# Performance work log

Measured on AMD Instinct MI355X. Metric: run time of the kernel, lower is better.

## Reference

```python
import jax, jax.numpy as jnp
import numpy as np

B, T, C = 16, 512, 32
W = 128            # max_window
SERIES_LEN = 100000
WIN_MIN, WIN_MAX = 2.0, 64.0
SHARP = 1.0        # fixed sharpness of the soft window edge
BN_EPS = 1e-5


def setup_inputs() -> dict:
    key = jax.random.key(0)
    ks = jax.random.split(key, 6)
    x = jax.random.normal(ks[0], (B, T, C), jnp.float32)
    full_series = jax.random.normal(ks[1], (SERIES_LEN, C), jnp.float32)
    # starts >= W so the lookback window never needs padding; end = start + T
    starts = jax.random.randint(ks[2], (B,), W, SERIES_LEN - T)
    indices = jnp.stack([starts, starts + T], axis=1).astype(jnp.int32)  # (B, 2)
    # raw (logit-space) per-channel window sizes, as in the torch init
    raw_win_mean = jax.random.normal(ks[3], (C,), jnp.float32)
    raw_win_std = jax.random.normal(ks[4], (C,), jnp.float32)
    return dict(
        x=x, full_series=full_series, indices=indices,
        raw_win_mean=raw_win_mean, raw_win_std=raw_win_std,
        gamma_mean=jnp.ones((C,), jnp.float32), beta_mean=jnp.zeros((C,), jnp.float32),
        gamma_std=jnp.ones((C,), jnp.float32), beta_std=jnp.zeros((C,), jnp.float32),
    )


def _soft_window_weights(raw_win):
    # sigmoid-mapped window size in [WIN_MIN, WIN_MAX], per channel
    win = WIN_MIN + jax.nn.sigmoid(raw_win) * (WIN_MAX - WIN_MIN)          # (C,)
    age = jnp.arange(W, dtype=jnp.float32)[::-1]                            # slot W-1 is most recent (age 0)
    w = jax.nn.sigmoid(SHARP * (win[None, :] - age[:, None]))               # (W, C)
    return w


def _rolling_windows(full_series, starts):
    # batch_windows[b] = full_series[starts[b]-W : starts[b]+T]   -> (B, W+T, C)
    offs = jnp.arange(W + T)
    bw = full_series[(starts - W)[:, None] + offs[None, :]]                 # (B, W+T, C)
    # window for output step t covers slots [t, t+W) (the W points before the current step)
    tidx = jnp.arange(T)[:, None] + jnp.arange(W)[None, :]                  # (T, W)
    return bw[:, tidx, :]                                                   # (B, T, W, C)


def _batchnorm(f, gamma, beta):
    # BatchNorm1d over (B, C, T): normalize per channel over batch and time, biased var
    mean = f.mean(axis=(0, 1))
    var = ((f - mean) ** 2).mean(axis=(0, 1))
    return (f - mean) * jax.lax.rsqrt(var + BN_EPS) * gamma + beta


def reference(x, full_series, indices, raw_win_mean, raw_win_std,
              gamma_mean, beta_mean, gamma_std, beta_std):
    starts = indices[:, 0]
    xw = _rolling_windows(full_series, starts)                              # (B, T, W, C)

    # feature 1: soft-window weighted mean
    w1 = _soft_window_weights(raw_win_mean)                                 # (W, C)
    s1 = jnp.sum(w1, axis=0)                                                # (C,)
    f_mean = jnp.einsum('btwc,wc->btc', xw, w1) / s1                        # (B, T, C)

    # feature 2: soft-window weighted std
    w2 = _soft_window_weights(raw_win_std)
    s2 = jnp.sum(w2, axis=0)
    m2 = jnp.einsum('btwc,wc->btc', xw, w2) / s2
    var2 = jnp.einsum('btwc,wc->btc', (xw - m2[:, :, None, :]) ** 2, w2) / s2
    f_std = jnp.sqrt(var2 + 1e-8)

    out_mean = _batchnorm(f_mean, gamma_mean, beta_mean)
    out_std = _batchnorm(f_std, gamma_std, beta_std)
    return jnp.concatenate([x, out_mean, out_std], axis=-1)                 # (B, T, 3*C)
```

## Files before the change

kernel.cpp:

```cpp
#include <hip/hip_runtime.h>
#include <math.h>

#define NB 16
#define NT 512
#define NC 32
#define NW 128
#define TILE_T 32
#define NTILES (NT / TILE_T)
#define NBLK (NB * NTILES)
#define NROWS (TILE_T + NW)
#define WIN_MIN_F 2.0f
#define WIN_RANGE_F 62.0f
#define EINV_F 0.36787944117f

#define WS_FMEAN 0
#define WS_FSTD  (NB*NT*NC)
#define WS_PART  (2*NB*NT*NC)

typedef float v2f __attribute__((ext_vector_type(2)));

__device__ __forceinline__ float fast_sigmoid_neg(float a) {
    return __builtin_amdgcn_rcpf(1.0f + __expf(a));
}
__device__ __forceinline__ v2f pk_fma(v2f a, v2f b, v2f c) {
    return __builtin_elementwise_fma(a, b, c);
}

__global__ __launch_bounds__(256) void feat_main(
    const float* __restrict__ x,
    const float* __restrict__ series,
    const int*   __restrict__ indices,
    const float* __restrict__ rwm,
    const float* __restrict__ rws,
    float* __restrict__ f_mean,
    float* __restrict__ f_std,
    float* __restrict__ partials,
    float* __restrict__ out)
{
    __shared__ __align__(16) float s_x [NROWS * NC];
    __shared__ __align__(16) float s_w1[NW * NC];
    __shared__ __align__(16) float s_w2[NW * NC];
    __shared__ float s_win[2 * NC];
    __shared__ __align__(16) float s_red[4 * 16 * NC];

    const int tid = threadIdx.x;
    const int blk = blockIdx.x;
    const int b   = blk >> 4;
    const int tt  = blk & 15;
    const int t0  = tt * TILE_T;
    const int start = indices[2 * b];

    {
        const int row = b * NT + t0 + (tid >> 3);
        const int q = tid & 7;
        ((float4*)out)[row * 24 + q] = ((const float4*)x)[row * 8 + q];
    }

    if (tid < 2 * NC) {
        const float raw = (tid < NC) ? rwm[tid] : rws[tid - NC];
        s_win[tid] = WIN_MIN_F + WIN_RANGE_F * fast_sigmoid_neg(-raw);
    }

    const float4* src4 = (const float4*)(series + (size_t)(start - NW + t0) * NC);
    float4* dst4 = (float4*)s_x;
#pragma unroll
    for (int k = 0; k < 5; ++k) {
        const int j = tid + k * 256;
        dst4[j] = src4[j];
    }
    __syncthreads();

    {
        const int c  = tid & 31;
        const int wc = tid >> 5;
        const int w0 = wc * 16;
        const float age0 = (float)(NW - 1 - w0);
        float E1 = __expf(age0 - s_win[c]);
        float E2 = __expf(age0 - s_win[NC + c]);
#pragma unroll
        for (int j = 0; j < 16; ++j) {
            const int idx = (w0 + j) * NC + c;
            s_w1[idx] = __builtin_amdgcn_rcpf(1.0f + E1);
            s_w2[idx] = __builtin_amdgcn_rcpf(1.0f + E2);
            E1 *= EINV_F;
            E2 *= EINV_F;
        }
    }
    __syncthreads();

    const int cp = tid & 15;
    const int tg = tid >> 4;
    const int r0 = tg * 2;

    const v2f* xv  = (const v2f*)s_x;
    const v2f* w1v = (const v2f*)s_w1;
    const v2f* w2v = (const v2f*)s_w2;

    v2f a1_0 = {0.f,0.f}, a2_0 = {0.f,0.f}, a3_0 = {0.f,0.f};
    v2f a1_1 = {0.f,0.f}, a2_1 = {0.f,0.f}, a3_1 = {0.f,0.f};
    v2f sw1 = {0.f,0.f}, sw2 = {0.f,0.f};

    v2f x0 = xv[(r0 + 0) * 16 + cp];
    v2f x1 = xv[(r0 + 1) * 16 + cp];
    v2f q0 = x0 * x0;
    v2f q1 = x1 * x1;

#pragma unroll 4
    for (int w = 0; w < NW; ++w) {
        const v2f wv1 = w1v[w * 16 + cp];
        const v2f wv2 = w2v[w * 16 + cp];
        sw1 = sw1 + wv1;
        sw2 = sw2 + wv2;
        a1_0 = pk_fma(x0, wv1, a1_0);
        a2_0 = pk_fma(x0, wv2, a2_0);
        a3_0 = pk_fma(q0, wv2, a3_0);
        a1_1 = pk_fma(x1, wv1, a1_1);
        a2_1 = pk_fma(x1, wv2, a2_1);
        a3_1 = pk_fma(q1, wv2, a3_1);
        const v2f xn = xv[(r0 + 2 + w) * 16 + cp];
        x0 = x1; q0 = q1;
        x1 = xn; q1 = xn * xn;
    }

    v2f inv1, inv2;
    inv1.x = __builtin_amdgcn_rcpf(sw1.x); inv1.y = __builtin_amdgcn_rcpf(sw1.y);
    inv2.x = __builtin_amdgcn_rcpf(sw2.x); inv2.y = __builtin_amdgcn_rcpf(sw2.y);

    v2f p0 = {0.f,0.f}, p1 = {0.f,0.f}, p2 = {0.f,0.f}, p3 = {0.f,0.f};
#pragma unroll
    for (int k = 0; k < 2; ++k) {
        const v2f A1 = k ? a1_1 : a1_0;
        const v2f A2 = k ? a2_1 : a2_0;
        const v2f A3 = k ? a3_1 : a3_0;
        const v2f fm = A1 * inv1;
        const v2f m2 = A2 * inv2;
        const v2f e2 = A3 * inv2;
        v2f fs;
        fs.x = sqrtf(fmaxf(e2.x - m2.x * m2.x, 0.f) + 1e-8f);
        fs.y = sqrtf(fmaxf(e2.y - m2.y * m2.y, 0.f) + 1e-8f);
        const int row = t0 + r0 + k;
        const size_t o2 = ((size_t)b * NT + row) * 16 + cp;
        ((v2f*)f_mean)[o2] = fm;
        ((v2f*)f_std)[o2]  = fs;
        p0 = p0 + fm;
        p1 = pk_fma(fm, fm, p1);
        p2 = p2 + fs;
        p3 = pk_fma(fs, fs, p3);
    }

    v2f* redv = (v2f*)s_red;
    redv[(0 * 16 + tg) * 16 + cp] = p0;
    redv[(1 * 16 + tg) * 16 + cp] = p1;
    redv[(2 * 16 + tg) * 16 + cp] = p2;
    redv[(3 * 16 + tg) * 16 + cp] = p3;
    __syncthreads();

    if (tid < 64) {
        const int stat = tid >> 4, cc = tid & 15;
        v2f s = {0.f, 0.f};
#pragma unroll
        for (int g = 0; g < 16; ++g)
            s = s + redv[(stat * 16 + g) * 16 + cc];
        ((v2f*)partials)[blk * 64 + stat * 16 + cc] = s;
    }
}

__global__ __launch_bounds__(256) void bn_write(
    const float* __restrict__ f_mean,
    const float* __restrict__ f_std,
    const float* __restrict__ partials,
    const float* __restrict__ gm, const float* __restrict__ bm,
    const float* __restrict__ gs, const float* __restrict__ bs,
    float* __restrict__ out)
{
    __shared__ __align__(16) float s_part[8 * 128];
    __shared__ __align__(16) float s_sums[128];
    __shared__ __align__(16) float s_coef[4 * NC];

    const int tid = threadIdx.x;

    {
        const int cell  = tid & 31;
        const int slice = tid >> 5;
        const float4* p4 = (const float4*)partials;
        float4 acc = {0.f, 0.f, 0.f, 0.f};
#pragma unroll 8
        for (int i = 0; i < 32; ++i) {
            const float4 v = p4[(slice * 32 + i) * 32 + cell];
            acc.x += v.x; acc.y += v.y; acc.z += v.z; acc.w += v.w;
        }
        *(float4*)&s_part[(slice * 32 + cell) * 4] = acc;
    }
    __syncthreads();
    if (tid < 32) {
        float4 s = {0.f, 0.f, 0.f, 0.f};
#pragma unroll
        for (int sl = 0; sl < 8; ++sl) {
            const float4 v = ((const float4*)s_part)[sl * 32 + tid];
            s.x += v.x; s.y += v.y; s.z += v.z; s.w += v.w;
        }
        ((float4*)s_sums)[tid] = s;
    }
    __syncthreads();
    if (tid < NC) {
        const float invN = 1.0f / (float)(NB * NT);
        const float mu_m  = s_sums[tid] * invN;
        float var_m = s_sums[32 + tid] * invN - mu_m * mu_m;
        var_m = fmaxf(var_m, 0.0f);
        const float A1 = gm[tid] / sqrtf(var_m + 1e-5f);
        const float B1 = bm[tid] - mu_m * A1;
        const float mu_s  = s_sums[64 + tid] * invN;
        float var_s = s_sums[96 + tid] * invN - mu_s * mu_s;
        var_s = fmaxf(var_s, 0.0f);
        const float A2 = gs[tid] / sqrtf(var_s + 1e-5f);
        const float B2 = bs[tid] - mu_s * A2;
        s_coef[tid]          = A1;
        s_coef[NC + tid]     = B1;
        s_coef[2 * NC + tid] = A2;
        s_coef[3 * NC + tid] = B2;
    }
    __syncthreads();

    const float4* fm4 = (const float4*)f_mean;
    const float4* fs4 = (const float4*)f_std;
    const float4* cf4 = (const float4*)s_coef;
    float4* out4 = (float4*)out;
    const int row0 = blockIdx.x * 32;

#pragma unroll
    for (int k = 0; k < 2; ++k) {
        const int j = tid + k * 256;
        const int r = j >> 4;
        const int q = j & 15;
        const int row = row0 + r;
        float4 v;
        int oq;
        if (q < 8) {
            const float4 f = fm4[row * 8 + q];
            const float4 A = cf4[q], Bv = cf4[8 + q];
            v.x = fmaf(f.x, A.x, Bv.x); v.y = fmaf(f.y, A.y, Bv.y);
            v.z = fmaf(f.z, A.z, Bv.z); v.w = fmaf(f.w, A.w, Bv.w);
            oq = 8 + q;
        } else {
            const int m = q - 8;
            const float4 f = fs4[row * 8 + m];
            const float4 A = cf4[16 + m], Bv = cf4[24 + m];
            v.x = fmaf(f.x, A.x, Bv.x); v.y = fmaf(f.y, A.y, Bv.y);
            v.z = fmaf(f.z, A.z, Bv.z); v.w = fmaf(f.w, A.w, Bv.w);
            oq = 16 + m;
        }
        out4[row * 24 + oq] = v;
    }
}

extern "C" void kernel_launch(void* const* d_in, const int* in_sizes, int n_in,
                              void* d_out, int out_size, void* d_ws, size_t ws_size,
                              hipStream_t stream) {
    const float* x      = (const float*)d_in[0];
    const float* series = (const float*)d_in[1];
    const int*   idx    = (const int*)d_in[2];
    const float* rwm    = (const float*)d_in[3];
    const float* rws    = (const float*)d_in[4];
    const float* gm     = (const float*)d_in[5];
    const float* bm     = (const float*)d_in[6];
    const float* gs     = (const float*)d_in[7];
    const float* bs     = (const float*)d_in[8];
    float* out = (float*)d_out;
    float* ws  = (float*)d_ws;

    float* f_mean   = ws + WS_FMEAN;
    float* f_std    = ws + WS_FSTD;
    float* partials = ws + WS_PART;

    feat_main<<<NBLK, 256, 0, stream>>>(x, series, idx, rwm, rws, f_mean, f_std, partials, out);
    bn_write<<<NBLK, 256, 0, stream>>>(f_mean, f_std, partials, gm, bm, gs, bs, out);
}
```

Baseline: 17.29 us.

## Split window across thread halves, 4 rows per thread, interleaved weights

Each thread now accumulates 4 output rows over half of the 128-tap window instead of 2 rows over the full window, and the two halves are combined through shared memory. The two weight tables are interleaved so one float4 LDS load fetches both weights, and the x tile is padded to a stride of 36 floats to reduce bank conflicts. The aim is fewer LDS loads per FMA and a shorter serial loop. The cost is extra syncs, a shared-memory merge step, and half the threads sitting idle during the epilogue.

Result: faster. 15.70 us (-9.2%).

```diff
diff --git a/kernel.cpp b/kernel.cpp
--- a/kernel.cpp
+++ b/kernel.cpp
@@ -9,6 +9,7 @@
 #define NTILES (NT / TILE_T)
 #define NBLK (NB * NTILES)
 #define NROWS (TILE_T + NW)
+#define XS 36
 #define WIN_MIN_F 2.0f
 #define WIN_RANGE_F 62.0f
 #define EINV_F 0.36787944117f
@@ -25,6 +26,10 @@
 __device__ __forceinline__ v2f pk_fma(v2f a, v2f b, v2f c) {
     return __builtin_elementwise_fma(a, b, c);
 }
+
+#define U_M    0
+#define U_SWH  3072
+#define U_RED  3200
 
 __global__ __launch_bounds__(256) void feat_main(
     const float* __restrict__ x,
@@ -37,11 +42,9 @@
     float* __restrict__ partials,
     float* __restrict__ out)
 {
-    __shared__ __align__(16) float s_x [NROWS * NC];
-    __shared__ __align__(16) float s_w1[NW * NC];
-    __shared__ __align__(16) float s_w2[NW * NC];
+    __shared__ __align__(16) float s_x[NROWS * XS];
+    __shared__ __align__(16) float s_u[NW * 64];
     __shared__ float s_win[2 * NC];
-    __shared__ __align__(16) float s_red[4 * 16 * NC];
 
     const int tid = threadIdx.x;
     const int blk = blockIdx.x;
@@ -62,105 +65,141 @@
     }
 
     const float4* src4 = (const float4*)(series + (size_t)(start - NW + t0) * NC);
-    float4* dst4 = (float4*)s_x;
 #pragma unroll
     for (int k = 0; k < 5; ++k) {
         const int j = tid + k * 256;
-        dst4[j] = src4[j];
+        const int row = j >> 3, c4 = (j & 7) << 2;
+        *(float4*)&s_x[row * XS + c4] = src4[j];
     }
     __syncthreads();
 
     {
         const int c  = tid & 31;
         const int wc = tid >> 5;
-        const int w0 = wc * 16;
-        const float age0 = (float)(NW - 1 - w0);
+        const int w0t = wc * 16;
+        const float age0 = (float)(NW - 1 - w0t);
         float E1 = __expf(age0 - s_win[c]);
         float E2 = __expf(age0 - s_win[NC + c]);
 #pragma unroll
         for (int j = 0; j < 16; ++j) {
-            const int idx = (w0 + j) * NC + c;
-            s_w1[idx] = __builtin_amdgcn_rcpf(1.0f + E1);
-            s_w2[idx] = __builtin_amdgcn_rcpf(1.0f + E2);
+            const int base = (w0t + j) * 64 + (c >> 1) * 4 + (c & 1);
+            s_u[base]     = __builtin_amdgcn_rcpf(1.0f + E1);
+            s_u[base + 2] = __builtin_amdgcn_rcpf(1.0f + E2);
             E1 *= EINV_F;
             E2 *= EINV_F;
         }
     }
     __syncthreads();
 
-    const int cp = tid & 15;
-    const int tg = tid >> 4;
-    const int r0 = tg * 2;
-
-    const v2f* xv  = (const v2f*)s_x;
-    const v2f* w1v = (const v2f*)s_w1;
-    const v2f* w2v = (const v2f*)s_w2;
-
-    v2f a1_0 = {0.f,0.f}, a2_0 = {0.f,0.f}, a3_0 = {0.f,0.f};
-    v2f a1_1 = {0.f,0.f}, a2_1 = {0.f,0.f}, a3_1 = {0.f,0.f};
+    const int cp   = tid & 15;
+    const int tg   = tid >> 4;
+    const int half = tg >> 3;
+    const int rg   = tg & 7;
+    const int r0   = rg * 4;
+    const int base = r0 + half * 64;
+
+    const v2f*    xv2 = (const v2f*)s_x;
+    const float4* wv4 = (const float4*)s_u;
+
+    v2f a1[4], a2[4], a3[4];
+#pragma unroll
+    for (int k = 0; k < 4; ++k) { a1[k] = (v2f){0.f,0.f}; a2[k] = (v2f){0.f,0.f}; a3[k] = (v2f){0.f,0.f}; }
     v2f sw1 = {0.f,0.f}, sw2 = {0.f,0.f};
 
-    v2f x0 = xv[(r0 + 0) * 16 + cp];
-    v2f x1 = xv[(r0 + 1) * 16 + cp];
-    v2f q0 = x0 * x0;
-    v2f q1 = x1 * x1;
-
+    v2f xs[4], qs[4];
+#pragma unroll
+    for (int k = 0; k < 4; ++k) {
+        xs[k] = xv2[(base + k) * 18 + cp];
+        qs[k] = xs[k] * xs[k];
+    }
+
+    const int w0 = half * 64;
 #pragma unroll 4
-    for (int w = 0; w < NW; ++w) {
-        const v2f wv1 = w1v[w * 16 + cp];
-        const v2f wv2 = w2v[w * 16 + cp];
-        sw1 = sw1 + wv1;
-        sw2 = sw2 + wv2;
-        a1_0 = pk_fma(x0, wv1, a1_0);
-        a2_0 = pk_fma(x0, wv2, a2_0);
-        a3_0 = pk_fma(q0, wv2, a3_0);
-        a1_1 = pk_fma(x1, wv1, a1_1);
-        a2_1 = pk_fma(x1, wv2, a2_1);
-        a3_1 = pk_fma(q1, wv2, a3_1);
-        const v2f xn = xv[(r0 + 2 + w) * 16 + cp];
-        x0 = x1; q0 = q1;
-        x1 = xn; q1 = xn * xn;
-    }
-
-    v2f inv1, inv2;
-    inv1.x = __builtin_amdgcn_rcpf(sw1.x); inv1.y = __builtin_amdgcn_rcpf(sw1.y);
-    inv2.x = __builtin_amdgcn_rcpf(sw2.x); inv2.y = __builtin_amdgcn_rcpf(sw2.y);
-
-    v2f p0 = {0.f,0.f}, p1 = {0.f,0.f}, p2 = {0.f,0.f}, p3 = {0.f,0.f};
-#pragma unroll
-    for (int k = 0; k < 2; ++k) {
-        const v2f A1 = k ? a1_1 : a1_0;
-        const v2f A2 = k ? a2_1 : a2_0;
-        const v2f A3 = k ? a3_1 : a3_0;
-        const v2f fm = A1 * inv1;
-        const v2f m2 = A2 * inv2;
-        const v2f e2 = A3 * inv2;
-        v2f fs;
-        fs.x = sqrtf(fmaxf(e2.x - m2.x * m2.x, 0.f) + 1e-8f);
-        fs.y = sqrtf(fmaxf(e2.y - m2.y * m2.y, 0.f) + 1e-8f);
-        const int row = t0 + r0 + k;
-        const size_t o2 = ((size_t)b * NT + row) * 16 + cp;
-        ((v2f*)f_mean)[o2] = fm;
-        ((v2f*)f_std)[o2]  = fs;
-        p0 = p0 + fm;
-        p1 = pk_fma(fm, fm, p1);
-        p2 = p2 + fs;
-        p3 = pk_fma(fs, fs, p3);
-    }
-
-    v2f* redv = (v2f*)s_red;
-    redv[(0 * 16 + tg) * 16 + cp] = p0;
-    redv[(1 * 16 + tg) * 16 + cp] = p1;
-    redv[(2 * 16 + tg) * 16 + cp] = p2;
-    redv[(3 * 16 + tg) * 16 + cp] = p3;
+    for (int i = 0; i < 64; ++i) {
+        const float4 wv = wv4[(w0 + i) * 16 + cp];
+        const v2f wlo = {wv.x, wv.y};
+        const v2f whi = {wv.z, wv.w};
+        sw1 = sw1 + wlo;
+        sw2 = sw2 + whi;
+#pragma unroll
+        for (int k = 0; k < 4; ++k) {
+            a1[k] = pk_fma(xs[k], wlo, a1[k]);
+            a2[k] = pk_fma(xs[k], whi, a2[k]);
+            a3[k] = pk_fma(qs[k], whi, a3[k]);
+        }
+        const v2f xn = xv2[(base + i + 4) * 18 + cp];
+        xs[0] = xs[1]; qs[0] = qs[1];
+        xs[1] = xs[2]; qs[1] = qs[2];
+        xs[2] = xs[3]; qs[2] = qs[3];
+        xs[3] = xn;    qs[3] = xn * xn;
+    }
+
+    __syncthreads();
+
+    v2f* s_m   = (v2f*)&s_u[U_M];
+    v2f* s_swh = (v2f*)&s_u[U_SWH];
+    v2f* s_red = (v2f*)&s_u[U_RED];
+
+    if (half) {
+        v2f* m = &s_m[(rg * 16 + cp) * 12];
+#pragma unroll
+        for (int k = 0; k < 4; ++k) {
+            m[k]     = a1[k];
+            m[4 + k] = a2[k];
+            m[8 + k] = a3[k];
+        }
+        if (rg == 0) {
+            s_swh[cp * 2]     = sw1;
+            s_swh[cp * 2 + 1] = sw2;
+        }
+    }
+    __syncthreads();
+
+    if (!half) {
+        const v2f* m = &s_m[(rg * 16 + cp) * 12];
+#pragma unroll
+        for (int k = 0; k < 4; ++k) {
+            a1[k] = a1[k] + m[k];
+            a2[k] = a2[k] + m[4 + k];
+            a3[k] = a3[k] + m[8 + k];
+        }
+        sw1 = sw1 + s_swh[cp * 2];
+        sw2 = sw2 + s_swh[cp * 2 + 1];
+
+        v2f inv1, inv2;
+        inv1.x = __builtin_amdgcn_rcpf(sw1.x); inv1.y = __builtin_amdgcn_rcpf(sw1.y);
+        inv2.x = __builtin_amdgcn_rcpf(sw2.x); inv2.y = __builtin_amdgcn_rcpf(sw2.y);
+
+        v2f p0 = {0.f,0.f}, p1 = {0.f,0.f}, p2 = {0.f,0.f}, p3 = {0.f,0.f};
+#pragma unroll
+        for (int k = 0; k < 4; ++k) {
+            const v2f fm = a1[k] * inv1;
+            const v2f m2 = a2[k] * inv2;
+            const v2f e2 = a3[k] * inv2;
+            v2f fs;
+            fs.x = sqrtf(fmaxf(e2.x - m2.x * m2.x, 0.f) + 1e-8f);
+            fs.y = sqrtf(fmaxf(e2.y - m2.y * m2.y, 0.f) + 1e-8f);
+            const size_t o2 = ((size_t)(b * NT + t0 + r0 + k)) * 16 + cp;
+            ((v2f*)f_mean)[o2] = fm;
+            ((v2f*)f_std)[o2]  = fs;
+            p0 = p0 + fm;
+            p1 = pk_fma(fm, fm, p1);
+            p2 = p2 + fs;
+            p3 = pk_fma(fs, fs, p3);
+        }
+        s_red[(0 * 8 + rg) * 16 + cp] = p0;
+        s_red[(1 * 8 + rg) * 16 + cp] = p1;
+        s_red[(2 * 8 + rg) * 16 + cp] = p2;
+        s_red[(3 * 8 + rg) * 16 + cp] = p3;
+    }
     __syncthreads();
 
     if (tid < 64) {
         const int stat = tid >> 4, cc = tid & 15;
         v2f s = {0.f, 0.f};
 #pragma unroll
-        for (int g = 0; g < 16; ++g)
-            s = s + redv[(stat * 16 + g) * 16 + cc];
+        for (int g = 0; g < 8; ++g)
+            s = s + s_red[(stat * 8 + g) * 16 + cc];
         ((v2f*)partials)[blk * 64 + stat * 16 + cc] = s;
     }
 }
```
